# Kernel tuning notes

Hardware: AMD Instinct MI355X
Metric: run time of the kernel (lower is better)

The kernel has to match this reference:

```python
import jax, jax.numpy as jnp
import numpy as np
from jax import lax

S, B, C = 7, 2, 20
W, H = 448.0, 448.0
IOU_THR = 0.1
PROB_THR = 8e-25
BATCH = 16
L = S * S * C + S * S * B + S * S * B * 4  # 1470
N = S * S * B * C                          # 1960 (box,class) candidates per image


def setup_inputs() -> dict:
    key = jax.random.key(0)
    prediction = jax.random.uniform(key, (BATCH, L), dtype=jnp.float32)
    return {"prediction": prediction}


def _pairwise_iou(b):
    # b: [N,4] boxes as (x_center, y_center, w, h); faithful to YoloDetector.iou
    x, y, w, h = b[:, 0], b[:, 1], b[:, 2], b[:, 3]
    tb = (jnp.minimum(x[:, None] + 0.5 * w[:, None], x[None, :] + 0.5 * w[None, :])
          - jnp.maximum(x[:, None] - 0.5 * w[:, None], x[None, :] - 0.5 * w[None, :]))
    lr = (jnp.minimum(y[:, None] + 0.5 * h[:, None], y[None, :] + 0.5 * h[None, :])
          - jnp.maximum(y[:, None] - 0.5 * h[:, None], y[None, :] - 0.5 * h[None, :]))
    inter = jnp.where((tb < 0) | (lr < 0), 0.0, tb * lr)
    area = w * h
    return inter / (area[:, None] + area[None, :] - inter)


def _decode_one(pred):
    # split flat prediction as in traDim(mode=3)
    SC, SB = S * S * C, S * S * B
    class_prob = pred[:SC].reshape(S, S, C)
    confidence = pred[SC:SC + SB].reshape(S, S, B)
    boxes = pred[SC + SB:].reshape(S, S, B, 4)

    # grid offsets: boxes[...,0] += row index i, boxes[...,1] += col index j
    idx = jnp.arange(S, dtype=pred.dtype)
    x = (boxes[..., 0] + idx[:, None, None]) / S * W
    y = (boxes[..., 1] + idx[None, :, None]) / S * H
    w = boxes[..., 2] * boxes[..., 2] * W
    h = boxes[..., 3] * boxes[..., 3] * H
    boxes_xywh = jnp.stack([x, y, w, h], axis=-1)          # [S,S,B,4]

    # eProbs[i,j,b,c] = classProb[i,j,c] * confidence[i,j,b]
    e_probs = class_prob[:, :, None, :] * confidence[:, :, :, None]  # [S,S,B,C]
    mask = e_probs >= PROB_THR
    # original uses argmax over the boolean mask along class axis for the class id
    cls = jnp.argmax(mask, axis=3)                         # [S,S,B]

    # flatten all (cell, box, class) candidates; below-threshold probs -> 0 (masking
    # replaces the data-dependent boolean filtering of the original)
    probs = jnp.where(mask, e_probs, 0.0).reshape(-1)                          # [N]
    boxes_c = jnp.broadcast_to(boxes_xywh[:, :, :, None, :], (S, S, B, C, 4)).reshape(-1, 4)
    cls_c = jnp.broadcast_to(cls[:, :, :, None], (S, S, B, C)).reshape(-1)     # [N]

    order = jnp.argsort(-probs)                            # descending by prob
    probs = probs[order]
    boxes_c = boxes_c[order]
    cls_c = cls_c[order]

    iou = _pairwise_iou(boxes_c)                           # [N,N], memory-dominant

    def step(p, xs):
        row, i = xs
        pivot = p[i]
        sup = (jnp.arange(N) > i) & (row > IOU_THR) & (pivot > 0)
        return jnp.where(sup, 0.0, p), None

    probs_nms, _ = lax.scan(step, probs, (iou, jnp.arange(N)))
    return boxes_c, probs_nms, cls_c


def reference(prediction):
    # returns (boxes [BATCH,N,4], probs_after_nms [BATCH,N], class_ids [BATCH,N]);
    # suppressed / sub-threshold candidates carry prob == 0 (fixed-shape analogue of
    # the original's boolean filtering)
    return jax.vmap(_decode_one)(prediction)
```

## Files before the change

### kernel.cpp

```cpp
#include <hip/hip_runtime.h>


constexpr int S_  = 7;
constexpr int Cc  = 20;
constexpr int NBOX  = 98;
constexpr int NENT  = 1960;
constexpr int NPAD  = 2048;
constexpr int LPRED = 1470;
constexpr int BATCH = 16;
constexpr float IOU_THR_  = 0.1f;
constexpr float PROB_THR_ = 8e-25f;

__device__ __forceinline__ unsigned long long rl64(unsigned long long v, int l)
{
    unsigned lo = (unsigned)__builtin_amdgcn_readlane((int)(unsigned)v, l);
    unsigned hi = (unsigned)__builtin_amdgcn_readlane((int)(unsigned)(v >> 32), l);
    return ((unsigned long long)hi << 32) | lo;
}

__global__ __launch_bounds__(1024)
void yolo_nms_kernel(const float* __restrict__ pred_all, float* __restrict__ out)
{
    const int b    = blockIdx.x;
    const int tid  = threadIdx.x;
    const int wid  = tid >> 6, lane = tid & 63;
    const float* pred = pred_all + b * LPRED;

    __shared__ float s_pred[LPRED];
    __shared__ unsigned long long s_k[NPAD];
    __shared__ float bXh[NBOX], bXl[NBOX], bYh[NBOX], bYl[NBOX], bA[NBOX];
    __shared__ float4 bBox[NBOX];
    __shared__ int   bCls[NBOX];
    __shared__ unsigned long long iouRow[NBOX * 2];
    __shared__ int firstpos[NBOX];
    __shared__ int boxorder[NBOX];
    __shared__ int kept[NBOX];
    __shared__ int s_nvalid;

    for (int i = tid; i < LPRED; i += 1024) s_pred[i] = pred[i];
    if (tid == 0) s_nvalid = 0;
    if (tid < NBOX) { kept[tid] = 0; firstpos[tid] = 0x7FFFFFFF; }
    __syncthreads();

    if (tid < NBOX) {
        const int bo = tid, cell = bo >> 1;
        const int ci = cell / S_, cj = cell % S_;
        const float bx = s_pred[1078 + bo * 4 + 0];
        const float by = s_pred[1078 + bo * 4 + 1];
        const float bw = s_pred[1078 + bo * 4 + 2];
        const float bh = s_pred[1078 + bo * 4 + 3];
        const float x = (bx + (float)ci) / 7.0f * 448.0f;
        const float y = (by + (float)cj) / 7.0f * 448.0f;
        const float w = bw * bw * 448.0f;
        const float h = bh * bh * 448.0f;
        bBox[bo] = make_float4(x, y, w, h);
        bXh[bo] = x + 0.5f * w;  bXl[bo] = x - 0.5f * w;
        bYh[bo] = y + 0.5f * h;  bYl[bo] = y - 0.5f * h;
        bA[bo]  = w * h;
        const float conf = s_pred[980 + bo];
        int cls = 0;
        for (int c = 0; c < Cc; ++c)
            if (s_pred[cell * Cc + c] * conf >= PROB_THR_) { cls = c; break; }
        bCls[bo] = cls;
    }

    for (int e = tid; e < NPAD; e += 1024) {
        unsigned long long key = 0ull;
        if (e < NENT) {
            const int bo = e / Cc, c = e - bo * Cc, cell = bo >> 1;
            const float ep = s_pred[cell * Cc + c] * s_pred[980 + bo];
            key = (unsigned long long)(0xFFFFFFFFu - (unsigned)e);
            if (ep >= PROB_THR_)
                key |= ((unsigned long long)__float_as_uint(ep) << 32);
        }
        s_k[e] = key;
    }
    __syncthreads();

    for (int r = wid; r < NBOX; r += 16) {
        const float rXh = bXh[r], rXl = bXl[r], rYh = bYh[r], rYl = bYl[r], rA = bA[r];
        bool s1 = false, s2 = false;
        {
            const int j = lane;
            const float tb = fminf(rXh, bXh[j]) - fmaxf(rXl, bXl[j]);
            const float lr = fminf(rYh, bYh[j]) - fmaxf(rYl, bYl[j]);
            const float inter = (tb < 0.0f || lr < 0.0f) ? 0.0f : tb * lr;
            const float iou = inter / (rA + bA[j] - inter);
            s1 = (iou > IOU_THR_);
        }
        if (lane + 64 < NBOX) {
            const int j = lane + 64;
            const float tb = fminf(rXh, bXh[j]) - fmaxf(rXl, bXl[j]);
            const float lr = fminf(rYh, bYh[j]) - fmaxf(rYl, bYl[j]);
            const float inter = (tb < 0.0f || lr < 0.0f) ? 0.0f : tb * lr;
            const float iou = inter / (rA + bA[j] - inter);
            s2 = (iou > IOU_THR_);
        }
        const unsigned long long m1 = __ballot(s1);
        const unsigned long long m2 = __ballot(s2);
        if (lane == 0) { iouRow[r * 2] = m1; iouRow[r * 2 + 1] = m2; }
    }

    for (int k = 2; k <= NPAD; k <<= 1) {
        for (int js = k >> 1; js > 0; js >>= 1) {
            if (js >= 128) __syncthreads();
            const int idx = ((tid & ~(js - 1)) << 1) | (tid & (js - 1));
            const int l   = idx | js;
            const unsigned long long a = s_k[idx], c = s_k[l];
            const bool dir = ((idx & k) == 0);
            if ((a < c) == dir) { s_k[idx] = c; s_k[l] = a; }
            if (js == 128) __syncthreads();
            else if (js < 128) asm volatile("s_waitcnt lgkmcnt(0)" ::: "memory");
        }
    }
    __syncthreads();

    for (int kp = tid; kp < NENT; kp += 1024) {
        const unsigned long long key = s_k[kp];
        if (key >> 32)
            atomicMin(&firstpos[(int)(0xFFFFFFFFu - (unsigned)key) / Cc], kp);
    }
    __syncthreads();

    if (tid < NBOX) {
        const int fp = firstpos[tid];
        if (fp != 0x7FFFFFFF) {
            int r = 0;
            for (int b2 = 0; b2 < NBOX; ++b2) r += (firstpos[b2] < fp) ? 1 : 0;
            boxorder[r] = tid;
            atomicAdd(&s_nvalid, 1);
        }
    }
    __syncthreads();

    if (tid < 64) {
        const int nv = s_nvalid;
        int bb0 = -1, bb1 = -1;
        unsigned long long r00 = 0, r01 = 0, r10 = 0, r11 = 0;
        if (tid < nv) {
            bb0 = boxorder[tid];
            r00 = iouRow[bb0 * 2]; r01 = iouRow[bb0 * 2 + 1];
        }
        if (tid + 64 < nv) {
            bb1 = boxorder[tid + 64];
            r10 = iouRow[bb1 * 2]; r11 = iouRow[bb1 * 2 + 1];
        }
        unsigned long long sup0 = 0, sup1 = 0, k0 = 0, k1 = 0;
        for (int r = 0; r < nv; ++r) {
            int bb; unsigned long long rw0, rw1;
            if (r < 64) {
                bb  = __builtin_amdgcn_readlane(bb0, r);
                rw0 = rl64(r00, r); rw1 = rl64(r01, r);
            } else {
                bb  = __builtin_amdgcn_readlane(bb1, r - 64);
                rw0 = rl64(r10, r - 64); rw1 = rl64(r11, r - 64);
            }
            const bool supped = (bb < 64) ? ((sup0 >> bb) & 1ull)
                                          : ((sup1 >> (bb - 64)) & 1ull);
            if (!supped) {
                if (bb < 64) k0 |= 1ull << bb; else k1 |= 1ull << (bb - 64);
                sup0 |= rw0; sup1 |= rw1;
            }
        }
        kept[tid] = (int)((k0 >> tid) & 1ull);
        if (tid < NBOX - 64) kept[tid + 64] = (int)((k1 >> tid) & 1ull);
    }
    __syncthreads();

    float* outBoxes = out + b * (NENT * 4);
    float* outProbs = out + BATCH * NENT * 4 + b * NENT;
    float* outCls   = out + BATCH * NENT * 5 + b * NENT;
    for (int kp = tid; kp < NENT; kp += 1024) {
        const unsigned long long key = s_k[kp];
        const unsigned pb2 = (unsigned)(key >> 32);
        const int idx = (int)(0xFFFFFFFFu - (unsigned)key);
        const int bo  = idx / Cc;
        *reinterpret_cast<float4*>(outBoxes + kp * 4) = bBox[bo];
        outProbs[kp] = (pb2 != 0u && kp == firstpos[bo] && kept[bo])
                         ? __uint_as_float(pb2) : 0.0f;
        outCls[kp] = (float)bCls[bo];
    }
}

extern "C" void kernel_launch(void* const* d_in, const int* in_sizes, int n_in,
                              void* d_out, int out_size, void* d_ws, size_t ws_size,
                              hipStream_t stream)
{
    const float* pred = (const float*)d_in[0];
    float* out = (float*)d_out;
    yolo_nms_kernel<<<BATCH, 1024, 0, stream>>>(pred, out);
}
```

Baseline: 36.08 us.

## Register-resident bitonic sort with 8 keys per thread and 256-thread blocks

Each thread now holds 8 sort keys in registers. The intra-thread bitonic stages run as register compare-exchanges, and only the cross-thread stages go through shared memory, with barriers required only when partners span waves. The block size drops from 1024 to 256 threads, which cuts barrier cost and shared-memory traffic per sort step. In exchange, each thread does more serial work and uses more registers, and the output stores are no longer coalesced across threads.

```diff
diff --git a/kernel.cpp b/kernel.cpp
--- a/kernel.cpp
+++ b/kernel.cpp
@@ -8,6 +8,7 @@
 constexpr int NPAD  = 2048;
 constexpr int LPRED = 1470;
 constexpr int BATCH = 16;
+constexpr int NT    = 256;
 constexpr float IOU_THR_  = 0.1f;
 constexpr float PROB_THR_ = 8e-25f;
 
@@ -18,7 +19,7 @@
     return ((unsigned long long)hi << 32) | lo;
 }
 
-__global__ __launch_bounds__(1024)
+__global__ __launch_bounds__(256)
 void yolo_nms_kernel(const float* __restrict__ pred_all, float* __restrict__ out)
 {
     const int b    = blockIdx.x;
@@ -27,7 +28,7 @@
     const float* pred = pred_all + b * LPRED;
 
     __shared__ float s_pred[LPRED];
-    __shared__ unsigned long long s_k[NPAD];
+    __shared__ unsigned long long ex[NPAD];
     __shared__ float bXh[NBOX], bXl[NBOX], bYh[NBOX], bYl[NBOX], bA[NBOX];
     __shared__ float4 bBox[NBOX];
     __shared__ int   bCls[NBOX];
@@ -37,7 +38,7 @@
     __shared__ int kept[NBOX];
     __shared__ int s_nvalid;
 
-    for (int i = tid; i < LPRED; i += 1024) s_pred[i] = pred[i];
+    for (int i = tid; i < LPRED; i += NT) s_pred[i] = pred[i];
     if (tid == 0) s_nvalid = 0;
     if (tid < NBOX) { kept[tid] = 0; firstpos[tid] = 0x7FFFFFFF; }
     __syncthreads();
@@ -64,20 +65,23 @@
         bCls[bo] = cls;
     }
 
-    for (int e = tid; e < NPAD; e += 1024) {
+    unsigned long long e[8];
+    #pragma unroll
+    for (int i = 0; i < 8; ++i) {
+        const int ee = tid * 8 + i;
         unsigned long long key = 0ull;
-        if (e < NENT) {
-            const int bo = e / Cc, c = e - bo * Cc, cell = bo >> 1;
+        if (ee < NENT) {
+            const int bo = ee / Cc, c = ee - bo * Cc, cell = bo >> 1;
             const float ep = s_pred[cell * Cc + c] * s_pred[980 + bo];
-            key = (unsigned long long)(0xFFFFFFFFu - (unsigned)e);
+            key = (unsigned long long)(0xFFFFFFFFu - (unsigned)ee);
             if (ep >= PROB_THR_)
                 key |= ((unsigned long long)__float_as_uint(ep) << 32);
         }
-        s_k[e] = key;
-    }
-    __syncthreads();
-
-    for (int r = wid; r < NBOX; r += 16) {
+        e[i] = key;
+    }
+    __syncthreads();
+
+    for (int r = wid; r < NBOX; r += 4) {
         const float rXh = bXh[r], rXl = bXl[r], rYh = bYh[r], rYl = bYl[r], rA = bA[r];
         bool s1 = false, s2 = false;
         {
@@ -101,24 +105,56 @@
         if (lane == 0) { iouRow[r * 2] = m1; iouRow[r * 2 + 1] = m2; }
     }
 
-    for (int k = 2; k <= NPAD; k <<= 1) {
-        for (int js = k >> 1; js > 0; js >>= 1) {
-            if (js >= 128) __syncthreads();
-            const int idx = ((tid & ~(js - 1)) << 1) | (tid & (js - 1));
-            const int l   = idx | js;
-            const unsigned long long a = s_k[idx], c = s_k[l];
-            const bool dir = ((idx & k) == 0);
-            if ((a < c) == dir) { s_k[idx] = c; s_k[l] = a; }
-            if (js == 128) __syncthreads();
-            else if (js < 128) asm volatile("s_waitcnt lgkmcnt(0)" ::: "memory");
-        }
-    }
-    __syncthreads();
-
-    for (int kp = tid; kp < NENT; kp += 1024) {
-        const unsigned long long key = s_k[kp];
-        if (key >> 32)
-            atomicMin(&firstpos[(int)(0xFFFFFFFFu - (unsigned)key) / Cc], kp);
+    auto CE = [&](int i, int j, bool desc) {
+        const unsigned long long a = e[i], c = e[j];
+        const unsigned long long mx = a > c ? a : c;
+        const unsigned long long mn = a > c ? c : a;
+        e[i] = desc ? mx : mn;
+        e[j] = desc ? mn : mx;
+    };
+
+    CE(0,1,true); CE(2,3,false); CE(4,5,true); CE(6,7,false);
+    CE(0,2,true); CE(1,3,true);  CE(4,6,false); CE(5,7,false);
+    CE(0,1,true); CE(2,3,true);  CE(4,5,false); CE(6,7,false);
+    {
+        const bool d8 = ((tid & 1) == 0);
+        CE(0,4,d8); CE(1,5,d8); CE(2,6,d8); CE(3,7,d8);
+        CE(0,2,d8); CE(1,3,d8); CE(4,6,d8); CE(5,7,d8);
+        CE(0,1,d8); CE(2,3,d8); CE(4,5,d8); CE(6,7,d8);
+    }
+
+    for (int k = 16; k <= NPAD; k <<= 1) {
+        const bool descT = ((tid & (k >> 3)) == 0);
+        for (int js = k >> 1; js >= 8; js >>= 1) {
+            const int jt = js >> 3;
+            const bool keep_max = (descT == ((tid & jt) == 0));
+            #pragma unroll
+            for (int i = 0; i < 8; ++i) ex[i * NT + tid] = e[i];
+            if (jt >= 64) __syncthreads();
+            else asm volatile("" ::: "memory");
+            const int pt = tid ^ jt;
+            unsigned long long p[8];
+            #pragma unroll
+            for (int i = 0; i < 8; ++i) p[i] = ex[i * NT + pt];
+            #pragma unroll
+            for (int i = 0; i < 8; ++i) {
+                const unsigned long long mx = e[i] > p[i] ? e[i] : p[i];
+                const unsigned long long mn = e[i] > p[i] ? p[i] : e[i];
+                e[i] = keep_max ? mx : mn;
+            }
+            if (jt >= 64) __syncthreads();
+            else asm volatile("" ::: "memory");
+        }
+        CE(0,4,descT); CE(1,5,descT); CE(2,6,descT); CE(3,7,descT);
+        CE(0,2,descT); CE(1,3,descT); CE(4,6,descT); CE(5,7,descT);
+        CE(0,1,descT); CE(2,3,descT); CE(4,5,descT); CE(6,7,descT);
+    }
+
+    #pragma unroll
+    for (int i = 0; i < 8; ++i) {
+        if (e[i] >> 32)
+            atomicMin(&firstpos[(int)(0xFFFFFFFFu - (unsigned)e[i]) / Cc],
+                      tid * 8 + i);
     }
     __syncthreads();
 
@@ -170,15 +206,19 @@
     float* outBoxes = out + b * (NENT * 4);
     float* outProbs = out + BATCH * NENT * 4 + b * NENT;
     float* outCls   = out + BATCH * NENT * 5 + b * NENT;
-    for (int kp = tid; kp < NENT; kp += 1024) {
-        const unsigned long long key = s_k[kp];
-        const unsigned pb2 = (unsigned)(key >> 32);
-        const int idx = (int)(0xFFFFFFFFu - (unsigned)key);
-        const int bo  = idx / Cc;
-        *reinterpret_cast<float4*>(outBoxes + kp * 4) = bBox[bo];
-        outProbs[kp] = (pb2 != 0u && kp == firstpos[bo] && kept[bo])
-                         ? __uint_as_float(pb2) : 0.0f;
-        outCls[kp] = (float)bCls[bo];
+    #pragma unroll
+    for (int i = 0; i < 8; ++i) {
+        const int kp = tid * 8 + i;
+        if (kp < NENT) {
+            const unsigned long long key = e[i];
+            const unsigned pb2 = (unsigned)(key >> 32);
+            const int idx = (int)(0xFFFFFFFFu - (unsigned)key);
+            const int bo  = idx / Cc;
+            *reinterpret_cast<float4*>(outBoxes + kp * 4) = bBox[bo];
+            outProbs[kp] = (pb2 != 0u && kp == firstpos[bo] && kept[bo])
+                             ? __uint_as_float(pb2) : 0.0f;
+            outCls[kp] = (float)bCls[bo];
+        }
     }
 }
 
@@ -188,5 +228,5 @@
 {
     const float* pred = (const float*)d_in[0];
     float* out = (float*)d_out;
-    yolo_nms_kernel<<<BATCH, 1024, 0, stream>>>(pred, out);
+    yolo_nms_kernel<<<BATCH, NT, 0, stream>>>(pred, out);
 }
```

Result: slower. 43.96 us (+21.8%).

## Replace bitonic sort with stable 4-pass LSD radix sort using wave ballots

Applied to the files above, without the earlier changes.

Swaps the 2048-element bitonic sort of packed 64-bit keys for a stable descending least-significant-digit radix sort over 8-bit digits of the 32-bit prob bits. Per-wave digit ranks come from ballot match masks, followed by a per-digit histogram prefix across waves and a block scan. This cuts the many barrier-separated compare-exchange stages down to four passes with a few barriers each, and the firstpos atomics are folded into the last scatter. The cost is extra shared memory for the ping-pong buffers and histograms, and ties must stay stable to keep index order.

```diff
diff --git a/kernel.cpp b/kernel.cpp
--- a/kernel.cpp
+++ b/kernel.cpp
@@ -23,21 +23,24 @@
 {
     const int b    = blockIdx.x;
     const int tid  = threadIdx.x;
-    const int wid  = tid >> 6, lane = tid & 63;
+    const int wv   = tid >> 6, lane = tid & 63;
+    const unsigned long long lt = (1ull << lane) - 1ull;
+    const unsigned long long le = lt | (1ull << lane);
     const float* pred = pred_all + b * LPRED;
 
     __shared__ float s_pred[LPRED];
-    __shared__ unsigned long long s_k[NPAD];
+    __shared__ unsigned int   sProb[2][NPAD];
+    __shared__ unsigned short sIdx [2][NPAD];
+    __shared__ alignas(16) unsigned short sHist[2][16 * 256];
+    __shared__ unsigned int   sTot[256];
     __shared__ float bXh[NBOX], bXl[NBOX], bYh[NBOX], bYl[NBOX], bA[NBOX];
     __shared__ float4 bBox[NBOX];
     __shared__ int   bCls[NBOX];
     __shared__ unsigned long long iouRow[NBOX * 2];
-    __shared__ int firstpos[NBOX];
-    __shared__ int boxorder[NBOX];
-    __shared__ int kept[NBOX];
-    __shared__ int s_nvalid;
+    __shared__ int firstpos[NBOX], boxorder[NBOX], kept[NBOX], s_nvalid;
 
     for (int i = tid; i < LPRED; i += 1024) s_pred[i] = pred[i];
+    reinterpret_cast<unsigned long long*>(sHist[0])[tid] = 0ull;
     if (tid == 0) s_nvalid = 0;
     if (tid < NBOX) { kept[tid] = 0; firstpos[tid] = 0x7FFFFFFF; }
     __syncthreads();
@@ -64,20 +67,21 @@
         bCls[bo] = cls;
     }
 
-    for (int e = tid; e < NPAD; e += 1024) {
-        unsigned long long key = 0ull;
+    #pragma unroll
+    for (int s = 0; s < 2; ++s) {
+        const int e = 2 * tid + s;
+        unsigned pb = 0u;
         if (e < NENT) {
             const int bo = e / Cc, c = e - bo * Cc, cell = bo >> 1;
             const float ep = s_pred[cell * Cc + c] * s_pred[980 + bo];
-            key = (unsigned long long)(0xFFFFFFFFu - (unsigned)e);
-            if (ep >= PROB_THR_)
-                key |= ((unsigned long long)__float_as_uint(ep) << 32);
-        }
-        s_k[e] = key;
-    }
-    __syncthreads();
-
-    for (int r = wid; r < NBOX; r += 16) {
+            if (ep >= PROB_THR_) pb = __float_as_uint(ep);
+        }
+        sProb[0][e] = pb;
+        sIdx[0][e]  = (unsigned short)e;
+    }
+    __syncthreads();
+
+    for (int r = wv; r < NBOX; r += 16) {
         const float rXh = bXh[r], rXl = bXl[r], rYh = bYh[r], rYl = bYl[r], rA = bA[r];
         bool s1 = false, s2 = false;
         {
@@ -101,26 +105,82 @@
         if (lane == 0) { iouRow[r * 2] = m1; iouRow[r * 2 + 1] = m2; }
     }
 
-    for (int k = 2; k <= NPAD; k <<= 1) {
-        for (int js = k >> 1; js > 0; js >>= 1) {
-            if (js >= 128) __syncthreads();
-            const int idx = ((tid & ~(js - 1)) << 1) | (tid & (js - 1));
-            const int l   = idx | js;
-            const unsigned long long a = s_k[idx], c = s_k[l];
-            const bool dir = ((idx & k) == 0);
-            if ((a < c) == dir) { s_k[idx] = c; s_k[l] = a; }
-            if (js == 128) __syncthreads();
-            else if (js < 128) asm volatile("s_waitcnt lgkmcnt(0)" ::: "memory");
-        }
-    }
-    __syncthreads();
-
-    for (int kp = tid; kp < NENT; kp += 1024) {
-        const unsigned long long key = s_k[kp];
-        if (key >> 32)
-            atomicMin(&firstpos[(int)(0xFFFFFFFFu - (unsigned)key) / Cc], kp);
-    }
-    __syncthreads();
+    int src = 0;
+    #pragma unroll
+    for (int pass = 0; pass < 4; ++pass) {
+        const int hb  = pass & 1;
+        const int dst = src ^ 1;
+        const int sh  = pass * 8;
+
+        const unsigned q0 = sProb[src][2 * tid];
+        const unsigned q1 = sProb[src][2 * tid + 1];
+        const unsigned short j0 = sIdx[src][2 * tid];
+        const unsigned short j1 = sIdx[src][2 * tid + 1];
+        const unsigned d0 = 0xFFu ^ ((q0 >> sh) & 0xFFu);
+        const unsigned d1 = 0xFFu ^ ((q1 >> sh) & 0xFFu);
+
+        unsigned long long mAA = ~0ull, mAB = ~0ull, mBA = ~0ull, mBB = ~0ull;
+        #pragma unroll
+        for (int bit = 0; bit < 8; ++bit) {
+            const unsigned long long ba = __ballot((d0 >> bit) & 1u);
+            const unsigned long long bb = __ballot((d1 >> bit) & 1u);
+            mAA &= ((d0 >> bit) & 1u) ? ba : ~ba;
+            mAB &= ((d0 >> bit) & 1u) ? bb : ~bb;
+            mBA &= ((d1 >> bit) & 1u) ? ba : ~ba;
+            mBB &= ((d1 >> bit) & 1u) ? bb : ~bb;
+        }
+        const int rank0 = __popcll(mAA & lt) + __popcll(mAB & lt);
+        const int rank1 = __popcll(mBA & le) + __popcll(mBB & lt);
+        sHist[hb][wv * 256 + d0] = (unsigned short)(__popcll(mAA) + __popcll(mAB));
+        sHist[hb][wv * 256 + d1] = (unsigned short)(__popcll(mBA) + __popcll(mBB));
+        __syncthreads();
+
+        if (tid < 256) {
+            unsigned run = 0;
+            unsigned short pf[16];
+            #pragma unroll
+            for (int w = 0; w < 16; ++w) {
+                const unsigned c = sHist[hb][w * 256 + tid];
+                pf[w] = (unsigned short)run;
+                run += c;
+            }
+            #pragma unroll
+            for (int w = 0; w < 16; ++w) sHist[hb][w * 256 + tid] = pf[w];
+            sTot[tid] = run;
+        }
+        __syncthreads();
+
+        if (wv == 0) {
+            const unsigned v0 = sTot[4 * lane],     v1 = sTot[4 * lane + 1];
+            const unsigned v2 = sTot[4 * lane + 2], v3 = sTot[4 * lane + 3];
+            const unsigned sm = v0 + v1 + v2 + v3;
+            unsigned inc = sm;
+            #pragma unroll
+            for (int off = 1; off < 64; off <<= 1) {
+                const unsigned t = __shfl_up(inc, off, 64);
+                if (lane >= off) inc += t;
+            }
+            const unsigned ex = inc - sm;
+            sTot[4 * lane]     = ex;
+            sTot[4 * lane + 1] = ex + v0;
+            sTot[4 * lane + 2] = ex + v0 + v1;
+            sTot[4 * lane + 3] = ex + v0 + v1 + v2;
+        }
+        __syncthreads();
+
+        const unsigned pos0 = sTot[d0] + sHist[hb][wv * 256 + d0] + (unsigned)rank0;
+        const unsigned pos1 = sTot[d1] + sHist[hb][wv * 256 + d1] + (unsigned)rank1;
+        sProb[dst][pos0] = q0;  sIdx[dst][pos0] = j0;
+        sProb[dst][pos1] = q1;  sIdx[dst][pos1] = j1;
+        if (pass == 3) {
+            if (q0) atomicMin(&firstpos[j0 / Cc], (int)pos0);
+            if (q1) atomicMin(&firstpos[j1 / Cc], (int)pos1);
+        } else {
+            reinterpret_cast<unsigned long long*>(sHist[hb ^ 1])[tid] = 0ull;
+        }
+        __syncthreads();
+        src = dst;
+    }
 
     if (tid < NBOX) {
         const int fp = firstpos[tid];
@@ -170,15 +230,18 @@
     float* outBoxes = out + b * (NENT * 4);
     float* outProbs = out + BATCH * NENT * 4 + b * NENT;
     float* outCls   = out + BATCH * NENT * 5 + b * NENT;
-    for (int kp = tid; kp < NENT; kp += 1024) {
-        const unsigned long long key = s_k[kp];
-        const unsigned pb2 = (unsigned)(key >> 32);
-        const int idx = (int)(0xFFFFFFFFu - (unsigned)key);
-        const int bo  = idx / Cc;
-        *reinterpret_cast<float4*>(outBoxes + kp * 4) = bBox[bo];
-        outProbs[kp] = (pb2 != 0u && kp == firstpos[bo] && kept[bo])
-                         ? __uint_as_float(pb2) : 0.0f;
-        outCls[kp] = (float)bCls[bo];
+    if (tid < NENT / 2) {
+        #pragma unroll
+        for (int s = 0; s < 2; ++s) {
+            const int kp = 2 * tid + s;
+            const unsigned q = sProb[0][kp];
+            const int j  = sIdx[0][kp];
+            const int bo = j / Cc;
+            *reinterpret_cast<float4*>(outBoxes + kp * 4) = bBox[bo];
+            outProbs[kp] = (q != 0u && kp == firstpos[bo] && kept[bo])
+                             ? __uint_as_float(q) : 0.0f;
+            outCls[kp] = (float)bCls[bo];
+        }
     }
 }
 
```

Result: faster. 32.58 us (-9.7%).

## Replace bitonic sort with rank-by-counting and split into two kernels

Applied to the files above, without the earlier changes.

Drops the 2048-element bitonic sort in shared memory. Each entry's sorted position is now computed by counting, via wave ballots, how many keys are larger or tied with a lower index. Per-box first position comes from a max-prob lookup plus a rank count. The box and class scatter moves to a second kernel spread over 256 blocks for more parallelism. The cost is a second launch, workspace round-trips, and O(N^2) ballot compares per image.

```diff
diff --git a/kernel.cpp b/kernel.cpp
--- a/kernel.cpp
+++ b/kernel.cpp
@@ -5,7 +5,7 @@
 constexpr int Cc  = 20;
 constexpr int NBOX  = 98;
 constexpr int NENT  = 1960;
-constexpr int NPAD  = 2048;
+constexpr int NKPAD = 1984;
 constexpr int LPRED = 1470;
 constexpr int BATCH = 16;
 constexpr float IOU_THR_  = 0.1f;
@@ -19,27 +19,30 @@
 }
 
 __global__ __launch_bounds__(1024)
-void yolo_nms_kernel(const float* __restrict__ pred_all, float* __restrict__ out)
-{
-    const int b    = blockIdx.x;
-    const int tid  = threadIdx.x;
-    const int wid  = tid >> 6, lane = tid & 63;
+void yolo_k1(const float* __restrict__ pred_all, float* __restrict__ out,
+             unsigned* __restrict__ wsKeys, float4* __restrict__ wsBox,
+             float* __restrict__ wsCls)
+{
+    const int b   = blockIdx.x;
+    const int tid = threadIdx.x;
+    const int wv  = tid >> 6, lane = tid & 63;
     const float* pred = pred_all + b * LPRED;
+    float* outProbs = out + BATCH * NENT * 4 + b * NENT;
 
     __shared__ float s_pred[LPRED];
-    __shared__ unsigned long long s_k[NPAD];
+    __shared__ unsigned sKey[NKPAD];
     __shared__ float bXh[NBOX], bXl[NBOX], bYh[NBOX], bYl[NBOX], bA[NBOX];
-    __shared__ float4 bBox[NBOX];
-    __shared__ int   bCls[NBOX];
+    __shared__ float bPmax[NBOX];
+    __shared__ unsigned bKmax[NBOX];
+    __shared__ int bEmax[NBOX];
     __shared__ unsigned long long iouRow[NBOX * 2];
-    __shared__ int firstpos[NBOX];
-    __shared__ int boxorder[NBOX];
-    __shared__ int kept[NBOX];
+    __shared__ int firstpos[NBOX], boxorder[NBOX];
     __shared__ int s_nvalid;
 
     for (int i = tid; i < LPRED; i += 1024) s_pred[i] = pred[i];
+    if (tid < NENT / 4)
+        reinterpret_cast<float4*>(outProbs)[tid] = make_float4(0.f, 0.f, 0.f, 0.f);
     if (tid == 0) s_nvalid = 0;
-    if (tid < NBOX) { kept[tid] = 0; firstpos[tid] = 0x7FFFFFFF; }
     __syncthreads();
 
     if (tid < NBOX) {
@@ -53,31 +56,43 @@
         const float y = (by + (float)cj) / 7.0f * 448.0f;
         const float w = bw * bw * 448.0f;
         const float h = bh * bh * 448.0f;
-        bBox[bo] = make_float4(x, y, w, h);
+        wsBox[b * NBOX + bo] = make_float4(x, y, w, h);
         bXh[bo] = x + 0.5f * w;  bXl[bo] = x - 0.5f * w;
         bYh[bo] = y + 0.5f * h;  bYl[bo] = y - 0.5f * h;
         bA[bo]  = w * h;
         const float conf = s_pred[980 + bo];
-        int cls = 0;
-        for (int c = 0; c < Cc; ++c)
-            if (s_pred[cell * Cc + c] * conf >= PROB_THR_) { cls = c; break; }
-        bCls[bo] = cls;
-    }
-
-    for (int e = tid; e < NPAD; e += 1024) {
-        unsigned long long key = 0ull;
-        if (e < NENT) {
-            const int bo = e / Cc, c = e - bo * Cc, cell = bo >> 1;
-            const float ep = s_pred[cell * Cc + c] * s_pred[980 + bo];
-            key = (unsigned long long)(0xFFFFFFFFu - (unsigned)e);
-            if (ep >= PROB_THR_)
-                key |= ((unsigned long long)__float_as_uint(ep) << 32);
-        }
-        s_k[e] = key;
-    }
-    __syncthreads();
-
-    for (int r = wid; r < NBOX; r += 16) {
+        float pm = 0.f; int em = 0; unsigned msk = 0u;
+        #pragma unroll
+        for (int c = 0; c < Cc; ++c) {
+            const float ep = s_pred[cell * Cc + c] * conf;
+            if (ep > pm) { pm = ep; em = c; }
+            if (ep >= PROB_THR_) msk |= 1u << c;
+        }
+        bPmax[bo] = pm;
+        bKmax[bo] = (pm >= PROB_THR_) ? __float_as_uint(pm) : 0u;
+        bEmax[bo] = bo * Cc + em;
+        wsCls[b * NBOX + bo] = (float)(msk ? (__ffs(msk) - 1) : 0);
+    }
+
+    {
+        const int e0 = 2 * tid, e1 = e0 + 1;
+        unsigned k0v = 0u, k1v = 0u;
+        if (e1 < NENT) {
+            const int bo0 = e0 / Cc, c0 = e0 - bo0 * Cc;
+            const int bo1 = e1 / Cc, c1 = e1 - bo1 * Cc;
+            const float ep0 = s_pred[(bo0 >> 1) * Cc + c0] * s_pred[980 + bo0];
+            const float ep1 = s_pred[(bo1 >> 1) * Cc + c1] * s_pred[980 + bo1];
+            if (ep0 >= PROB_THR_) k0v = __float_as_uint(ep0);
+            if (ep1 >= PROB_THR_) k1v = __float_as_uint(ep1);
+            *reinterpret_cast<unsigned long long*>(&wsKeys[b * NENT + e0]) =
+                ((unsigned long long)k1v << 32) | k0v;
+        }
+        if (e0 < NKPAD) sKey[e0] = k0v;
+        if (e1 < NKPAD) sKey[e1] = k1v;
+    }
+    __syncthreads();
+
+    for (int r = wv; r < NBOX; r += 16) {
         const float rXh = bXh[r], rXl = bXl[r], rYh = bYh[r], rYl = bYl[r], rA = bA[r];
         bool s1 = false, s2 = false;
         {
@@ -100,25 +115,22 @@
         const unsigned long long m2 = __ballot(s2);
         if (lane == 0) { iouRow[r * 2] = m1; iouRow[r * 2 + 1] = m2; }
     }
-
-    for (int k = 2; k <= NPAD; k <<= 1) {
-        for (int js = k >> 1; js > 0; js >>= 1) {
-            if (js >= 128) __syncthreads();
-            const int idx = ((tid & ~(js - 1)) << 1) | (tid & (js - 1));
-            const int l   = idx | js;
-            const unsigned long long a = s_k[idx], c = s_k[l];
-            const bool dir = ((idx & k) == 0);
-            if ((a < c) == dir) { s_k[idx] = c; s_k[l] = a; }
-            if (js == 128) __syncthreads();
-            else if (js < 128) asm volatile("s_waitcnt lgkmcnt(0)" ::: "memory");
-        }
-    }
-    __syncthreads();
-
-    for (int kp = tid; kp < NENT; kp += 1024) {
-        const unsigned long long key = s_k[kp];
-        if (key >> 32)
-            atomicMin(&firstpos[(int)(0xFFFFFFFFu - (unsigned)key) / Cc], kp);
+    for (int bo = wv; bo < NBOX; bo += 16) {
+        const unsigned km = bKmax[bo];
+        if (km == 0u) {
+            if (lane == 0) firstpos[bo] = 0x7FFFFFFF;
+        } else {
+            const int em = bEmax[bo];
+            int cnt = 0;
+            #pragma unroll
+            for (int it = 0; it < 31; ++it) {
+                const int j = lane + 64 * it;
+                const unsigned kj = sKey[j];
+                cnt += __popcll(__ballot(kj > km));
+                cnt += __popcll(__ballot(kj == km && j < em));
+            }
+            if (lane == 0) firstpos[bo] = cnt;
+        }
     }
     __syncthreads();
 
@@ -162,23 +174,53 @@
                 sup0 |= rw0; sup1 |= rw1;
             }
         }
-        kept[tid] = (int)((k0 >> tid) & 1ull);
-        if (tid < NBOX - 64) kept[tid + 64] = (int)((k1 >> tid) & 1ull);
-    }
-    __syncthreads();
-
-    float* outBoxes = out + b * (NENT * 4);
-    float* outProbs = out + BATCH * NENT * 4 + b * NENT;
-    float* outCls   = out + BATCH * NENT * 5 + b * NENT;
-    for (int kp = tid; kp < NENT; kp += 1024) {
-        const unsigned long long key = s_k[kp];
-        const unsigned pb2 = (unsigned)(key >> 32);
-        const int idx = (int)(0xFFFFFFFFu - (unsigned)key);
-        const int bo  = idx / Cc;
-        *reinterpret_cast<float4*>(outBoxes + kp * 4) = bBox[bo];
-        outProbs[kp] = (pb2 != 0u && kp == firstpos[bo] && kept[bo])
-                         ? __uint_as_float(pb2) : 0.0f;
-        outCls[kp] = (float)bCls[bo];
+        if ((k0 >> tid) & 1ull) outProbs[firstpos[tid]] = bPmax[tid];
+        if (tid + 64 < NBOX && ((k1 >> tid) & 1ull))
+            outProbs[firstpos[tid + 64]] = bPmax[tid + 64];
+    }
+}
+
+__global__ __launch_bounds__(1024)
+void yolo_k2(const unsigned* __restrict__ wsKeys, const float4* __restrict__ wsBox,
+             const float* __restrict__ wsCls, float* __restrict__ out)
+{
+    const int it    = blockIdx.x >> 4;
+    const int chunk = blockIdx.x & 15;
+    const int tid   = threadIdx.x;
+    const int wv    = tid >> 6, lane = tid & 63;
+
+    __shared__ unsigned sKey[NKPAD];
+    __shared__ float4 sBox[NBOX];
+    __shared__ float  sCls[NBOX];
+
+    for (int i = tid; i < NKPAD; i += 1024)
+        sKey[i] = (i < NENT) ? wsKeys[it * NENT + i] : 0u;
+    if (tid < NBOX) { sBox[tid] = wsBox[it * NBOX + tid]; sCls[tid] = wsCls[it * NBOX + tid]; }
+    __syncthreads();
+
+    unsigned kj[31];
+    #pragma unroll
+    for (int r = 0; r < 31; ++r) kj[r] = sKey[lane + 64 * r];
+
+    float* outBoxes = out + it * (NENT * 4);
+    float* outCls   = out + BATCH * NENT * 5 + it * NENT;
+
+    const int base = chunk * 123;
+    const int end  = min(NENT, base + 123);
+    for (int e = base + wv; e < end; e += 16) {
+        const unsigned ke = sKey[e];
+        int cnt = 0;
+        #pragma unroll
+        for (int r = 0; r < 31; ++r) {
+            const int j = lane + 64 * r;
+            cnt += __popcll(__ballot(kj[r] > ke));
+            cnt += __popcll(__ballot(kj[r] == ke && j < e));
+        }
+        if (lane == 0) {
+            const int bo = e / Cc;
+            *reinterpret_cast<float4*>(outBoxes + cnt * 4) = sBox[bo];
+            outCls[cnt] = sCls[bo];
+        }
     }
 }
 
@@ -188,5 +230,10 @@
 {
     const float* pred = (const float*)d_in[0];
     float* out = (float*)d_out;
-    yolo_nms_kernel<<<BATCH, 1024, 0, stream>>>(pred, out);
-}
+    unsigned* wsKeys = (unsigned*)d_ws;
+    float4*   wsBox  = (float4*)((char*)d_ws + (size_t)BATCH * NENT * 4);
+    float*    wsCls  = (float*)((char*)d_ws + (size_t)BATCH * NENT * 4
+                                            + (size_t)BATCH * NBOX * 16);
+    yolo_k1<<<BATCH, 1024, 0, stream>>>(pred, out, wsKeys, wsBox, wsCls);
+    yolo_k2<<<BATCH * 16, 1024, 0, stream>>>(wsKeys, wsBox, wsCls, out);
+}
```

Measured after the change: 57.86 us. 1.6x slower.
